# Performance work log

Measured on AMD Instinct MI355X. Metric: run time of the kernel, lower is better.

## Reference

```python
import jax, jax.numpy as jnp
import numpy as np

B, N, D = 2048, 64, 256
DH = D // 2  # theta/phi projection dim
EPS = 1e-5

def layer_norm(x, g, b):
    m = jnp.mean(x, axis=-1, keepdims=True)
    v = jnp.var(x, axis=-1, keepdims=True)
    return (x - m) * jax.lax.rsqrt(v + EPS) * g + b

def graph_conv(x, adj, th_w, ph_w, fc_w, fc_b):
    # static adjacency: softmax over rows, shared across batch
    A_static = jax.nn.softmax(adj, axis=-1)  # [N, N]
    q = jnp.einsum('bnd,hd->bnh', x, th_w)   # [B, N, DH]
    k = jnp.einsum('bnd,hd->bnh', x, ph_w)   # [B, N, DH]
    scores = jnp.einsum('bni,bmi->bnm', q, k) / jnp.sqrt(jnp.asarray(DH, x.dtype))
    A_hat = A_static[None] + jax.nn.softmax(scores, axis=-1)  # [B, N, N]
    agg = jnp.einsum('bnm,bmd->bnd', A_hat, x)
    return jnp.einsum('bnd,od->bno', agg, fc_w) + fc_b

def setup_inputs() -> dict:
    key = jax.random.key(0)
    ks = jax.random.split(key, 12)
    eye = jnp.eye(N, dtype=jnp.float32)
    s = 1.0 / np.sqrt(D)
    return {
        'graph':  jax.random.normal(ks[0], (B, N, D), jnp.float32),
        'ln_in_g': jnp.ones((D,), jnp.float32), 'ln_in_b': jnp.zeros((D,), jnp.float32),
        'adj0':  eye + 0.01 * jax.random.normal(ks[1], (N, N), jnp.float32),
        'th0':   jax.random.uniform(ks[2], (DH, D), jnp.float32, -s, s),
        'ph0':   jax.random.uniform(ks[3], (DH, D), jnp.float32, -s, s),
        'fcw0':  jax.random.uniform(ks[4], (D, D), jnp.float32, -s, s),
        'fcb0':  jax.random.uniform(ks[5], (D,), jnp.float32, -s, s),
        'ln0_g': jnp.ones((D,), jnp.float32), 'ln0_b': jnp.zeros((D,), jnp.float32),
        'adj1':  eye + 0.01 * jax.random.normal(ks[6], (N, N), jnp.float32),
        'th1':   jax.random.uniform(ks[7], (DH, D), jnp.float32, -s, s),
        'ph1':   jax.random.uniform(ks[8], (DH, D), jnp.float32, -s, s),
        'fcw1':  jax.random.uniform(ks[9], (D, D), jnp.float32, -s, s),
        'fcb1':  jax.random.uniform(ks[10], (D,), jnp.float32, -s, s),
    }

def reference(graph, ln_in_g, ln_in_b, adj0, th0, ph0, fcw0, fcb0,
              ln0_g, ln0_b, adj1, th1, ph1, fcw1, fcb1):
    x = layer_norm(graph, ln_in_g, ln_in_b)
    x = graph_conv(x, adj0, th0, ph0, fcw0, fcb0)
    x = layer_norm(x, ln0_g, ln0_b)
    x = jnp.where(x >= 0, x, 0.1 * x)  # LeakyReLU(0.1); dropout is identity in eval
    x = graph_conv(x, adj1, th1, ph1, fcw1, fcb1)
    return x
```

## Files before the change

kernel.cpp:

```cpp
#include <hip/hip_runtime.h>

typedef __bf16 bf16x8 __attribute__((ext_vector_type(8)));
typedef __bf16 bf16x4 __attribute__((ext_vector_type(4)));
typedef float  f32x4  __attribute__((ext_vector_type(4)));

constexpr int WS_AS0 = 0;
constexpr int WS_AS1 = 4096;
constexpr int WS_MT0 = 8192;
constexpr int WS_MT1 = 73728;
constexpr int WS_FC0 = 139264;
constexpr int WS_FC1 = 204800;

static __device__ __forceinline__ f32x4 mfma16(bf16x8 a, bf16x8 b, f32x4 c) {
    return __builtin_amdgcn_mfma_f32_16x16x32_bf16(a, b, c, 0, 0, 0);
}

__global__ void prep_all(const float* __restrict__ adj0, const float* __restrict__ adj1,
                         const float* __restrict__ th0,  const float* __restrict__ ph0,
                         const float* __restrict__ th1,  const float* __restrict__ ph1,
                         const float* __restrict__ fc0,  const float* __restrict__ fc1,
                         __bf16* __restrict__ wsb) {
    const int blk = blockIdx.x, tid = threadIdx.x;
    if (blk < 32) {
        const int w = tid >> 6, lane = tid & 63;
        const int row = blk * 4 + w;
        const int layer = row >> 6, r = row & 63;
        const float* a = (layer ? adj1 : adj0) + r * 64;
        const float v = a[lane];
        float mx = v;
        #pragma unroll
        for (int m = 1; m < 64; m <<= 1) mx = fmaxf(mx, __shfl_xor(mx, m));
        float e = __expf(v - mx), sum = e;
        #pragma unroll
        for (int m = 1; m < 64; m <<= 1) sum += __shfl_xor(sum, m);
        wsb[(layer ? WS_AS1 : WS_AS0) + r * 64 + lane] = (__bf16)(e / sum);
    } else if (blk < 544) {
        const int e = (blk - 32) & 255, layer = (blk - 32) >> 8, d = tid;
        const float* th = layer ? th1 : th0;
        const float* ph = layer ? ph1 : ph0;
        float s = 0.f;
        #pragma unroll 8
        for (int h = 0; h < 128; ++h) s += ph[h * 256 + e] * th[h * 256 + d];
        wsb[(layer ? WS_MT1 : WS_MT0) + e * 256 + d] = (__bf16)(s * 0.088388347648318447f);
    } else {
        const int i = (blk - 544) * 512 + tid * 2;
        if (i < 65536) {
            wsb[WS_FC0 + i]     = (__bf16)fc0[i];
            wsb[WS_FC0 + i + 1] = (__bf16)fc0[i + 1];
        } else {
            wsb[WS_FC1 + i - 65536] = (__bf16)fc1[i - 65536];
            wsb[WS_FC1 + i - 65535] = (__bf16)fc1[i - 65535];
        }
    }
}

__global__ __launch_bounds__(512, 4) void fused_gcn(
    const float* __restrict__ graph,
    const float* __restrict__ ln_in_g, const float* __restrict__ ln_in_b,
    const __bf16* __restrict__ wsb,
    const float* __restrict__ fcb0, const float* __restrict__ ln0_g,
    const float* __restrict__ ln0_b, const float* __restrict__ fcb1,
    float* __restrict__ outp)
{
    constexpr int XN_S = 264;
    constexpr int ZT_S = 72;
    constexpr int AH_S = 72;

    __shared__ __align__(16) __bf16 sXn[64 * XN_S];
    __shared__ __align__(16) __bf16 sR1[256 * ZT_S];
    __shared__ __align__(16) __bf16 sAh[64 * AH_S];
    __shared__ float sRed[128];

    const int tid = threadIdx.x;
    const int w = tid >> 6, lane = tid & 63;
    const int l15 = lane & 15, qd = lane >> 4;
    const int b = blockIdx.x;

    {
        if (tid < 128) sRed[tid] = 0.f;
        const int r = tid >> 3, ci = (tid & 7) * 32;
        const float* gp = graph + (size_t)b * 16384 + r * 256 + ci;
        f32x4 v[8];
        float s = 0.f, s2 = 0.f;
        #pragma unroll
        for (int j = 0; j < 8; ++j) {
            v[j] = *(const f32x4*)(gp + j * 4);
            #pragma unroll
            for (int e = 0; e < 4; ++e) { s += v[j][e]; s2 += v[j][e] * v[j][e]; }
        }
        #pragma unroll
        for (int m = 1; m <= 4; m <<= 1) { s += __shfl_xor(s, m); s2 += __shfl_xor(s2, m); }
        const float mean = s * (1.f / 256.f);
        const float var  = s2 * (1.f / 256.f) - mean * mean;
        const float rstd = rsqrtf(var + 1e-5f);
        #pragma unroll
        for (int j = 0; j < 8; ++j) {
            f32x4 gg = *(const f32x4*)(ln_in_g + ci + j * 4);
            f32x4 bb = *(const f32x4*)(ln_in_b + ci + j * 4);
            bf16x4 pk;
            #pragma unroll
            for (int e = 0; e < 4; ++e)
                pk[e] = (__bf16)((v[j][e] - mean) * rstd * gg[e] + bb[e]);
            *(bf16x4*)&sXn[r * XN_S + ci + j * 4] = pk;
        }
    }
    __syncthreads();

    #pragma unroll 1
    for (int layer = 0; layer < 2; ++layer) {
        const __bf16* As  = wsb + (layer ? WS_AS1 : WS_AS0);
        const __bf16* mtw = wsb + (layer ? WS_MT1 : WS_MT0);
        const __bf16* fcw = wsb + (layer ? WS_FC1 : WS_FC0);
        const float*  fcb = layer ? fcb1 : fcb0;

        {
            {
                const int r = tid >> 3, c8 = (tid & 7) * 8;
                *(bf16x8*)&sAh[r * AH_S + c8] = *(const bf16x8*)(As + r * 64 + c8);
            }
            const int row0 = w * 32 + l15;
            f32x4 tacc[2][4];
            #pragma unroll
            for (int i = 0; i < 4; ++i) {
                tacc[0][i] = (f32x4){0.f, 0.f, 0.f, 0.f};
                tacc[1][i] = (f32x4){0.f, 0.f, 0.f, 0.f};
            }
            #pragma unroll
            for (int kk = 0; kk < 8; ++kk) {
                const int co = kk * 32 + qd * 8;
                bf16x8 amt0 = *(const bf16x8*)(mtw + row0 * 256 + co);
                bf16x8 amt1 = *(const bf16x8*)(mtw + (row0 + 16) * 256 + co);
                #pragma unroll
                for (int nt = 0; nt < 4; ++nt) {
                    bf16x8 bx = *(const bf16x8*)&sXn[(nt * 16 + l15) * XN_S + co];
                    tacc[0][nt] = mfma16(amt0, bx, tacc[0][nt]);
                    tacc[1][nt] = mfma16(amt1, bx, tacc[1][nt]);
                }
            }
            #pragma unroll
            for (int jm = 0; jm < 2; ++jm)
                #pragma unroll
                for (int nt = 0; nt < 4; ++nt) {
                    bf16x4 pk;
                    #pragma unroll
                    for (int r = 0; r < 4; ++r) pk[r] = (__bf16)tacc[jm][nt][r];
                    *(bf16x4*)&sR1[(nt * 16 + l15) * XN_S + (w * 2 + jm) * 16 + qd * 4] = pk;
                }
        }
        __syncthreads();

        if (w < 4) {
            const int mb = w * 16;
            bf16x8 at[8];
            #pragma unroll
            for (int kk = 0; kk < 8; ++kk)
                at[kk] = *(const bf16x8*)&sR1[(mb + l15) * XN_S + kk * 32 + qd * 8];
            f32x4 sc[4];
            #pragma unroll
            for (int nt = 0; nt < 4; ++nt) sc[nt] = (f32x4){0.f, 0.f, 0.f, 0.f};
            #pragma unroll
            for (int nt = 0; nt < 4; ++nt)
                #pragma unroll
                for (int kk = 0; kk < 8; ++kk) {
                    bf16x8 bx = *(const bf16x8*)&sXn[(nt * 16 + l15) * XN_S + kk * 32 + qd * 8];
                    sc[nt] = mfma16(at[kk], bx, sc[nt]);
                }
            #pragma unroll
            for (int r = 0; r < 4; ++r) {
                float v[4];
                #pragma unroll
                for (int nt = 0; nt < 4; ++nt) v[nt] = sc[nt][r];
                float mx = fmaxf(fmaxf(v[0], v[1]), fmaxf(v[2], v[3]));
                #pragma unroll
                for (int m = 1; m <= 8; m <<= 1) mx = fmaxf(mx, __shfl_xor(mx, m));
                float e[4], sum = 0.f;
                #pragma unroll
                for (int nt = 0; nt < 4; ++nt) { e[nt] = __expf(v[nt] - mx); sum += e[nt]; }
                #pragma unroll
                for (int m = 1; m <= 8; m <<= 1) sum += __shfl_xor(sum, m);
                const float inv = 1.f / sum;
                const int row = mb + qd * 4 + r;
                #pragma unroll
                for (int nt = 0; nt < 4; ++nt) {
                    const int col = nt * 16 + l15;
                    const float as = (float)sAh[row * AH_S + col];
                    sAh[row * AH_S + col] = (__bf16)(e[nt] * inv + as);
                }
            }
        }
        __syncthreads();

        {
            const int o0 = w * 32 + l15;
            f32x4 zacc[4][2];
            #pragma unroll
            for (int m = 0; m < 4; ++m) {
                zacc[m][0] = (f32x4){0.f, 0.f, 0.f, 0.f};
                zacc[m][1] = (f32x4){0.f, 0.f, 0.f, 0.f};
            }
            #pragma unroll
            for (int kk = 0; kk < 8; ++kk) {
                const int co = kk * 32 + qd * 8;
                bf16x8 afc0 = *(const bf16x8*)(fcw + o0 * 256 + co);
                bf16x8 afc1 = *(const bf16x8*)(fcw + (o0 + 16) * 256 + co);
                #pragma unroll
                for (int m = 0; m < 4; ++m) {
                    bf16x8 ax = *(const bf16x8*)&sXn[(m * 16 + l15) * XN_S + co];
                    zacc[m][0] = mfma16(ax, afc0, zacc[m][0]);
                    zacc[m][1] = mfma16(ax, afc1, zacc[m][1]);
                }
            }
            #pragma unroll
            for (int jm = 0; jm < 2; ++jm) {
                const int o = w * 32 + jm * 16 + l15;
                #pragma unroll
                for (int m = 0; m < 4; ++m) {
                    bf16x4 pk;
                    #pragma unroll
                    for (int r = 0; r < 4; ++r) pk[r] = (__bf16)zacc[m][jm][r];
                    *(bf16x4*)&sR1[o * ZT_S + m * 16 + qd * 4] = pk;
                }
            }
        }
        __syncthreads();

        {
            const int mb = (w & 3) * 16, ng = w >> 2;
            bf16x8 aa[2];
            #pragma unroll
            for (int kk = 0; kk < 2; ++kk)
                aa[kk] = *(const bf16x8*)&sAh[(mb + l15) * AH_S + kk * 32 + qd * 8];
            f32x4 oacc[8];
            #pragma unroll
            for (int j = 0; j < 8; ++j) {
                const int o = ng * 128 + j * 16 + l15;
                f32x4 acc = {0.f, 0.f, 0.f, 0.f};
                #pragma unroll
                for (int kk = 0; kk < 2; ++kk) {
                    bf16x8 bb = *(const bf16x8*)&sR1[o * ZT_S + kk * 32 + qd * 8];
                    acc = mfma16(aa[kk], bb, acc);
                }
                const float bias = fcb[o];
                #pragma unroll
                for (int r = 0; r < 4; ++r) acc[r] += bias;
                oacc[j] = acc;
            }

            if (layer == 0) {
                #pragma unroll
                for (int r = 0; r < 4; ++r) {
                    float s = 0.f, s2 = 0.f;
                    #pragma unroll
                    for (int j = 0; j < 8; ++j) { const float vv = oacc[j][r]; s += vv; s2 += vv * vv; }
                    #pragma unroll
                    for (int m = 1; m <= 8; m <<= 1) { s += __shfl_xor(s, m); s2 += __shfl_xor(s2, m); }
                    if (l15 == 0) {
                        const int row = mb + qd * 4 + r;
                        atomicAdd(&sRed[row], s);
                        atomicAdd(&sRed[64 + row], s2);
                    }
                }
                __syncthreads();
                float mean4[4], rstd4[4];
                #pragma unroll
                for (int r = 0; r < 4; ++r) {
                    const int row = mb + qd * 4 + r;
                    const float mean = sRed[row] * (1.f / 256.f);
                    const float var  = sRed[64 + row] * (1.f / 256.f) - mean * mean;
                    mean4[r] = mean;
                    rstd4[r] = rsqrtf(var + 1e-5f);
                }
                #pragma unroll
                for (int j = 0; j < 8; ++j) {
                    const int o = ng * 128 + j * 16 + l15;
                    const float g = ln0_g[o], bb = ln0_b[o];
                    #pragma unroll
                    for (int r = 0; r < 4; ++r) {
                        float y = (oacc[j][r] - mean4[r]) * rstd4[r] * g + bb;
                        y = (y >= 0.f) ? y : 0.1f * y;
                        sXn[(mb + qd * 4 + r) * XN_S + o] = (__bf16)y;
                    }
                }
                __syncthreads();
            } else {
                float* op = outp + (size_t)b * 16384;
                #pragma unroll
                for (int j = 0; j < 8; ++j) {
                    const int o = ng * 128 + j * 16 + l15;
                    #pragma unroll
                    for (int r = 0; r < 4; ++r)
                        op[(mb + qd * 4 + r) * 256 + o] = oacc[j][r];
                }
            }
        }
    }
}

extern "C" void kernel_launch(void* const* d_in, const int* in_sizes, int n_in,
                              void* d_out, int out_size, void* d_ws, size_t ws_size,
                              hipStream_t stream) {
    const float* graph   = (const float*)d_in[0];
    const float* ln_in_g = (const float*)d_in[1];
    const float* ln_in_b = (const float*)d_in[2];
    const float* adj0    = (const float*)d_in[3];
    const float* th0     = (const float*)d_in[4];
    const float* ph0     = (const float*)d_in[5];
    const float* fcw0    = (const float*)d_in[6];
    const float* fcb0    = (const float*)d_in[7];
    const float* ln0_g   = (const float*)d_in[8];
    const float* ln0_b   = (const float*)d_in[9];
    const float* adj1    = (const float*)d_in[10];
    const float* th1     = (const float*)d_in[11];
    const float* ph1     = (const float*)d_in[12];
    const float* fcw1    = (const float*)d_in[13];
    const float* fcb1    = (const float*)d_in[14];
    __bf16* wsb = (__bf16*)d_ws;

    prep_all<<<800, 256, 0, stream>>>(adj0, adj1, th0, ph0, th1, ph1, fcw0, fcw1, wsb);
    fused_gcn<<<2048, 512, 0, stream>>>(graph, ln_in_g, ln_in_b, wsb,
                                        fcb0, ln0_g, ln0_b, fcb1, (float*)d_out);
}
```

Measured before the change: 399.7 us.

## Overlap FC projection with softmax and drop a barrier via wave-local output columns

Waves 4-7, which sat idle during the score/softmax stage, now compute their slice of the x·fc_w product in that stage, and waves 0-3 compute theirs after the barrier. The final A_hat·Z product is reorganized so each wave reads only the Z columns it wrote itself. That removes the barrier between writing Z and using it. The layer-1 path adds a trailing barrier so the next batch iteration does not overwrite shared memory too early. Extra packed registers held across the softmax stage may raise register pressure.

Result: slower. 503.6 us (+26.0%).

```diff
diff --git a/kernel.cpp b/kernel.cpp
--- a/kernel.cpp
+++ b/kernel.cpp
@@ -149,7 +149,39 @@
         }
         __syncthreads();
 
-        if (w < 4) {
+        bf16x4 zpk[4][2];
+        auto pz_compute = [&]() {
+            const int o0 = w * 32 + l15;
+            f32x4 zacc[4][2];
+            #pragma unroll
+            for (int m = 0; m < 4; ++m) {
+                zacc[m][0] = (f32x4){0.f, 0.f, 0.f, 0.f};
+                zacc[m][1] = (f32x4){0.f, 0.f, 0.f, 0.f};
+            }
+            #pragma unroll
+            for (int kk = 0; kk < 8; ++kk) {
+                const int co = kk * 32 + qd * 8;
+                bf16x8 afc0 = *(const bf16x8*)(fcw + o0 * 256 + co);
+                bf16x8 afc1 = *(const bf16x8*)(fcw + (o0 + 16) * 256 + co);
+                #pragma unroll
+                for (int m = 0; m < 4; ++m) {
+                    bf16x8 ax = *(const bf16x8*)&sXn[(m * 16 + l15) * XN_S + co];
+                    zacc[m][0] = mfma16(ax, afc0, zacc[m][0]);
+                    zacc[m][1] = mfma16(ax, afc1, zacc[m][1]);
+                }
+            }
+            #pragma unroll
+            for (int m = 0; m < 4; ++m)
+                #pragma unroll
+                for (int jm = 0; jm < 2; ++jm)
+                    #pragma unroll
+                    for (int r = 0; r < 4; ++r)
+                        zpk[m][jm][r] = (__bf16)zacc[m][jm][r];
+        };
+
+        if (w >= 4) {
+            pz_compute();
+        } else {
             const int mb = w * 16;
             bf16x8 at[8];
             #pragma unroll
@@ -190,107 +222,94 @@
         }
         __syncthreads();
 
+        if (w < 4) pz_compute();
+
         {
-            const int o0 = w * 32 + l15;
-            f32x4 zacc[4][2];
-            #pragma unroll
-            for (int m = 0; m < 4; ++m) {
-                zacc[m][0] = (f32x4){0.f, 0.f, 0.f, 0.f};
-                zacc[m][1] = (f32x4){0.f, 0.f, 0.f, 0.f};
-            }
-            #pragma unroll
-            for (int kk = 0; kk < 8; ++kk) {
-                const int co = kk * 32 + qd * 8;
-                bf16x8 afc0 = *(const bf16x8*)(fcw + o0 * 256 + co);
-                bf16x8 afc1 = *(const bf16x8*)(fcw + (o0 + 16) * 256 + co);
-                #pragma unroll
-                for (int m = 0; m < 4; ++m) {
-                    bf16x8 ax = *(const bf16x8*)&sXn[(m * 16 + l15) * XN_S + co];
-                    zacc[m][0] = mfma16(ax, afc0, zacc[m][0]);
-                    zacc[m][1] = mfma16(ax, afc1, zacc[m][1]);
-                }
-            }
             #pragma unroll
             for (int jm = 0; jm < 2; ++jm) {
                 const int o = w * 32 + jm * 16 + l15;
                 #pragma unroll
-                for (int m = 0; m < 4; ++m) {
-                    bf16x4 pk;
-                    #pragma unroll
-                    for (int r = 0; r < 4; ++r) pk[r] = (__bf16)zacc[m][jm][r];
-                    *(bf16x4*)&sR1[o * ZT_S + m * 16 + qd * 4] = pk;
-                }
-            }
-        }
-        __syncthreads();
-
-        {
-            const int mb = (w & 3) * 16, ng = w >> 2;
-            bf16x8 aa[2];
-            #pragma unroll
-            for (int kk = 0; kk < 2; ++kk)
-                aa[kk] = *(const bf16x8*)&sAh[(mb + l15) * AH_S + kk * 32 + qd * 8];
-            f32x4 oacc[8];
-            #pragma unroll
-            for (int j = 0; j < 8; ++j) {
-                const int o = ng * 128 + j * 16 + l15;
-                f32x4 acc = {0.f, 0.f, 0.f, 0.f};
-                #pragma unroll
-                for (int kk = 0; kk < 2; ++kk) {
-                    bf16x8 bb = *(const bf16x8*)&sR1[o * ZT_S + kk * 32 + qd * 8];
-                    acc = mfma16(aa[kk], bb, acc);
-                }
-                const float bias = fcb[o];
-                #pragma unroll
-                for (int r = 0; r < 4; ++r) acc[r] += bias;
-                oacc[j] = acc;
+                for (int m = 0; m < 4; ++m)
+                    *(bf16x4*)&sR1[o * ZT_S + m * 16 + qd * 4] = zpk[m][jm];
             }
 
             if (layer == 0) {
-                #pragma unroll
-                for (int r = 0; r < 4; ++r) {
-                    float s = 0.f, s2 = 0.f;
-                    #pragma unroll
-                    for (int j = 0; j < 8; ++j) { const float vv = oacc[j][r]; s += vv; s2 += vv * vv; }
-                    #pragma unroll
-                    for (int m = 1; m <= 8; m <<= 1) { s += __shfl_xor(s, m); s2 += __shfl_xor(s2, m); }
-                    if (l15 == 0) {
-                        const int row = mb + qd * 4 + r;
-                        atomicAdd(&sRed[row], s);
-                        atomicAdd(&sRed[64 + row], s2);
+                f32x4 oacc[4][2];
+                #pragma unroll
+                for (int jm = 0; jm < 2; ++jm) {
+                    const int o = w * 32 + jm * 16 + l15;
+                    bf16x8 bb0 = *(const bf16x8*)&sR1[o * ZT_S + qd * 8];
+                    bf16x8 bb1 = *(const bf16x8*)&sR1[o * ZT_S + 32 + qd * 8];
+                    const float bias = fcb[o];
+                    #pragma unroll
+                    for (int ng = 0; ng < 4; ++ng) {
+                        bf16x8 aa0 = *(const bf16x8*)&sAh[(ng * 16 + l15) * AH_S + qd * 8];
+                        bf16x8 aa1 = *(const bf16x8*)&sAh[(ng * 16 + l15) * AH_S + 32 + qd * 8];
+                        f32x4 acc = {0.f, 0.f, 0.f, 0.f};
+                        acc = mfma16(aa0, bb0, acc);
+                        acc = mfma16(aa1, bb1, acc);
+                        #pragma unroll
+                        for (int r = 0; r < 4; ++r) acc[r] += bias;
+                        oacc[ng][jm] = acc;
                     }
                 }
+                #pragma unroll
+                for (int ng = 0; ng < 4; ++ng)
+                    #pragma unroll
+                    for (int r = 0; r < 4; ++r) {
+                        float s  = oacc[ng][0][r] + oacc[ng][1][r];
+                        float s2 = oacc[ng][0][r] * oacc[ng][0][r]
+                                 + oacc[ng][1][r] * oacc[ng][1][r];
+                        #pragma unroll
+                        for (int m = 1; m <= 8; m <<= 1) {
+                            s += __shfl_xor(s, m); s2 += __shfl_xor(s2, m);
+                        }
+                        if (l15 == 0) {
+                            const int n = ng * 16 + qd * 4 + r;
+                            atomicAdd(&sRed[n], s);
+                            atomicAdd(&sRed[64 + n], s2);
+                        }
+                    }
                 __syncthreads();
-                float mean4[4], rstd4[4];
-                #pragma unroll
-                for (int r = 0; r < 4; ++r) {
-                    const int row = mb + qd * 4 + r;
-                    const float mean = sRed[row] * (1.f / 256.f);
-                    const float var  = sRed[64 + row] * (1.f / 256.f) - mean * mean;
-                    mean4[r] = mean;
-                    rstd4[r] = rsqrtf(var + 1e-5f);
-                }
-                #pragma unroll
-                for (int j = 0; j < 8; ++j) {
-                    const int o = ng * 128 + j * 16 + l15;
-                    const float g = ln0_g[o], bb = ln0_b[o];
+                const float g0 = ln0_g[w * 32 + l15],      gb0 = ln0_b[w * 32 + l15];
+                const float g1 = ln0_g[w * 32 + 16 + l15], gb1 = ln0_b[w * 32 + 16 + l15];
+                #pragma unroll
+                for (int ng = 0; ng < 4; ++ng)
                     #pragma unroll
                     for (int r = 0; r < 4; ++r) {
-                        float y = (oacc[j][r] - mean4[r]) * rstd4[r] * g + bb;
-                        y = (y >= 0.f) ? y : 0.1f * y;
-                        sXn[(mb + qd * 4 + r) * XN_S + o] = (__bf16)y;
+                        const int n = ng * 16 + qd * 4 + r;
+                        const float mean = sRed[n] * (1.f / 256.f);
+                        const float var  = sRed[64 + n] * (1.f / 256.f) - mean * mean;
+                        const float rstd = rsqrtf(var + 1e-5f);
+                        float y0 = (oacc[ng][0][r] - mean) * rstd * g0 + gb0;
+                        float y1 = (oacc[ng][1][r] - mean) * rstd * g1 + gb1;
+                        y0 = (y0 >= 0.f) ? y0 : 0.1f * y0;
+                        y1 = (y1 >= 0.f) ? y1 : 0.1f * y1;
+                        sXn[n * XN_S + w * 32 + l15]      = (__bf16)y0;
+                        sXn[n * XN_S + w * 32 + 16 + l15] = (__bf16)y1;
                     }
-                }
                 __syncthreads();
             } else {
                 float* op = outp + (size_t)b * 16384;
                 #pragma unroll
-                for (int j = 0; j < 8; ++j) {
-                    const int o = ng * 128 + j * 16 + l15;
-                    #pragma unroll
-                    for (int r = 0; r < 4; ++r)
-                        op[(mb + qd * 4 + r) * 256 + o] = oacc[j][r];
-                }
+                for (int jm = 0; jm < 2; ++jm) {
+                    const int o = w * 32 + jm * 16 + l15;
+                    bf16x8 bb0 = *(const bf16x8*)&sR1[o * ZT_S + qd * 8];
+                    bf16x8 bb1 = *(const bf16x8*)&sR1[o * ZT_S + 32 + qd * 8];
+                    const float bias = fcb[o];
+                    #pragma unroll
+                    for (int ng = 0; ng < 4; ++ng) {
+                        bf16x8 aa0 = *(const bf16x8*)&sAh[(ng * 16 + l15) * AH_S + qd * 8];
+                        bf16x8 aa1 = *(const bf16x8*)&sAh[(ng * 16 + l15) * AH_S + 32 + qd * 8];
+                        f32x4 acc = {0.f, 0.f, 0.f, 0.f};
+                        acc = mfma16(aa0, bb0, acc);
+                        acc = mfma16(aa1, bb1, acc);
+                        #pragma unroll
+                        for (int r = 0; r < 4; ++r)
+                            op[(ng * 16 + qd * 4 + r) * 256 + o] = acc[r] + bias;
+                    }
+                }
+                __syncthreads();
             }
         }
     }
```
